# Performance work log

Hardware: AMD Instinct MI355X
Metric: run time of the kernel (lower is better)

The kernel has to match this reference:

```python
import jax, jax.numpy as jnp
import numpy as np

K = 3
STRIDE = 1
PAD = 1
DIL = 1


def _unfold(a):
    # a: (N, C, H, W) -> patches (N, C, K*K, oH, oW), matching torch.F.unfold
    # channel-major ordering (c slowest, then kernel row, then kernel col).
    N, C, H, W = a.shape
    oH = (H + 2 * PAD - DIL * (K - 1) - 1) // STRIDE + 1
    oW = (W + 2 * PAD - DIL * (K - 1) - 1) // STRIDE + 1
    ap = jnp.pad(a, ((0, 0), (0, 0), (PAD, PAD), (PAD, PAD)))
    cols = []
    for i in range(K):
        for j in range(K):
            cols.append(ap[:, :,
                           i * DIL: i * DIL + (oH - 1) * STRIDE + 1: STRIDE,
                           j * DIL: j * DIL + (oW - 1) * STRIDE + 1: STRIDE])
    return jnp.stack(cols, axis=2)  # (N, C, K*K, oH, oW)


def setup_inputs() -> dict:
    key = jax.random.key(0)
    k1, k2, k3, k4, k5 = jax.random.split(key, 5)
    N, C, O, H, W = 4, 128, 256, 128, 128
    x = jax.random.normal(k1, (N, C, H, W), dtype=jnp.float32)
    depth = jax.random.uniform(k2, (N, 1, H, W), dtype=jnp.float32)
    camera_params = jax.random.normal(k3, (N, 4), dtype=jnp.float32)
    weight = jax.random.normal(k4, (O, C, K, K), dtype=jnp.float32) * 0.05
    bias = jax.random.normal(k5, (O,), dtype=jnp.float32) * 0.05
    return {"x": x, "depth": depth, "camera_params": camera_params,
            "weight": weight, "bias": bias}


def reference(x, depth, camera_params, weight, bias):
    # camera_params is accepted but unused, mirroring the torch module.
    O, C = weight.shape[0], weight.shape[1]
    xp = _unfold(x)        # (N, C, kk, oH, oW)
    dp = _unfold(depth)    # (N, 1, kk, oH, oW)
    w = weight.reshape(O, C, K * K)
    # depth-modulated im2col GEMM: sum_{c,p} w[o,c,p] * x_patch * d_patch
    out = jnp.einsum('ocp,ncpxy->noxy', w, xp * dp)
    return out + bias[None, :, None, None]
```

## Files before the change

### kernel.cpp

```cpp
#include <hip/hip_runtime.h>
#include <stdint.h>


#define C_IN 128
#define O_OUT 256
#define HW 128
#define NB 4
#define PADW 130

#define XD_ELEMS ((size_t)NB * PADW * PADW * C_IN)
#define XD_BYTES (XD_ELEMS * 2)
#define WT_ELEMS ((size_t)O_OUT * C_IN * 9)
#define WT_BYTES (WT_ELEMS * 2)

typedef __attribute__((ext_vector_type(8))) short short8;
typedef __attribute__((ext_vector_type(4))) float f32x4;
typedef __attribute__((ext_vector_type(2))) float f32x2;
typedef __attribute__((ext_vector_type(4))) unsigned uint4v;

__device__ __forceinline__ unsigned f2bf_bits(float f) {
  unsigned u = __builtin_bit_cast(unsigned, f);
  return (u + 0x7fffu + ((u >> 16) & 1u)) >> 16;
}

__device__ __forceinline__ void async_load16(const void* g, void* l) {
  __builtin_amdgcn_global_load_lds(
      (__attribute__((address_space(1))) void*)g,
      (__attribute__((address_space(3))) void*)l, 16, 0, 0);
}

__global__ __launch_bounds__(256) void prep_all(const float* __restrict__ x,
                                                const float* __restrict__ depth,
                                                const float* __restrict__ w,
                                                short* __restrict__ xd,
                                                short* __restrict__ wt2) {
  const int R = blockIdx.x;
  const int tid = threadIdx.x;

  if (R >= NB * HW + NB) {
    int gid = (R - (NB * HW + NB)) * 4608 + tid;
#pragma unroll
    for (int i = 0; i < 18; ++i, gid += 256) {
      const int j = gid & 7;
      const int lane = (gid >> 3) & 63;
      const int T = (gid >> 9) & 7;
      const int g2 = gid >> 12;
      const int s = g2 % 36;
      const int o0 = g2 / 36;
      const int ln = lane & 15, q = lane >> 4;
      const int o = (o0 << 7) + (T << 4) + ln;
      const int cc = s / 9;
      const int tap = s % 9;
      const int c = (cc << 5) + (q << 3) + j;
      wt2[gid] = (short)f2bf_bits(w[((size_t)o * C_IN + c) * 9 + tap]);
    }
    return;
  }

  if (R >= NB * HW) {
    const int n = R - NB * HW;
    uint4v* base0 = (uint4v*)(xd + (size_t)n * PADW * PADW * C_IN);
    uint4v* base1 = (uint4v*)(xd + ((size_t)n * PADW + (PADW - 1)) * PADW * C_IN);
    const uint4v z = {0u, 0u, 0u, 0u};
    const int per_row = PADW * C_IN * 2 / 16;
    for (int i = tid; i < per_row; i += 256) {
      base0[i] = z;
      base1[i] = z;
    }
    return;
  }

  __shared__ short s[C_IN * PADW];

  const int n = R >> 7, y = R & 127;
  const int lane = tid & 63;
  const int wave = tid >> 6;

  {
    unsigned* row = (unsigned*)(xd + ((size_t)(n * PADW + y + 1) * PADW) * C_IN);
    if (tid < 64) row[tid] = 0u;
    else if (tid < 128) row[(size_t)(PADW - 1) * 64 + (tid - 64)] = 0u;
  }

  const f32x2 d2 = *(const f32x2*)(depth + ((size_t)n * HW + y) * HW + 2 * lane);
  const float* xrow = x + (((size_t)n * C_IN) * HW + y) * HW + 2 * lane;
  unsigned* s32 = (unsigned*)s;
#pragma unroll 8
  for (int ci = 0; ci < 32; ++ci) {
    const int c = ci * 4 + wave;
    const f32x2 v = *(const f32x2*)(xrow + (size_t)c * HW * HW);
    s32[c * 65 + lane] = f2bf_bits(v.x * d2.x) | (f2bf_bits(v.y * d2.y) << 16);
  }
  __syncthreads();

  const unsigned short* s16 = (const unsigned short*)s;
  unsigned* orow = (unsigned*)(xd + ((size_t)(n * PADW + y + 1) * PADW + 1) * C_IN);
#pragma unroll 8
  for (int i = 0; i < 32; ++i) {
    const int flat = tid + i * 256;
    const int px = flat >> 6, cp = flat & 63;
    const unsigned lo = s16[(2 * cp) * PADW + px];
    const unsigned hi = s16[(2 * cp + 1) * PADW + px];
    orow[flat] = lo | (hi << 16);
  }
}

__global__ __launch_bounds__(256, 2) void conv_mfma(
    const short* __restrict__ xd, const short* __restrict__ wt2,
    const float* __restrict__ bias, float* __restrict__ out) {
  __shared__ __align__(16) short xbuf[2][16640];

  const int tid = threadIdx.x;
  const int bx = blockIdx.x;
  const int n = bx >> 6;
  const int y = (bx & 63) << 1;
  const int o0b = blockIdx.y;
  const int lane = tid & 63;
  const int wave = tid >> 6;
  const int wm = wave & 1, wn = wave >> 1;
  const int ln = lane & 15, q = lane >> 4;

  const short* wbase = wt2 + (size_t)o0b * 147456 + (wm << 11) + (lane << 3);

  const short* xsrc0 = xd + (size_t)(n * PADW + y) * PADW * C_IN +
                       (tid >> 2) * C_IN + ((tid & 3) ^ ((tid >> 3) & 3)) * 8;

  f32x4 acc[4][8] = {};
  short8 areg[2][4];

  auto loadA = [&](int s, int p) {
#pragma unroll
    for (int t = 0; t < 4; ++t)
      areg[p][t] = *(const short8*)(wbase + (size_t)s * 4096 + t * 512);
  };

  {
    short* xdst = &xbuf[0][0] + tid * 8;
#pragma unroll
    for (int j = 0; j < 8; ++j)
      async_load16(xsrc0 + j * 8192, xdst + j * 2048);
    if (tid < 32) async_load16(xsrc0 + 8 * 8192, xdst + 8 * 2048);
  }
  loadA(0, 0);
  __syncthreads();

#pragma unroll
  for (int cc = 0; cc < 4; ++cc) {
#pragma unroll
    for (int tap = 0; tap < 9; ++tap) {
      const int s = cc * 9 + tap;
      if (s + 1 < 36) loadA(s + 1, (s + 1) & 1);

      if (cc + 1 < 4) {
        const short* sp = xsrc0 + ((cc + 1) << 5);
        short* xdst = &xbuf[(cc + 1) & 1][0] + tid * 8;
        if (tap < 8) async_load16(sp + tap * 8192, xdst + tap * 2048);
        if (tap == 0 && tid < 32)
          async_load16(sp + 8 * 8192, xdst + 8 * 2048);
      }

      const int ti = tap / 3, tj = tap % 3;
      const int rbase = (wn + ti) * 130 + tj;

      short8 b[8];
#pragma unroll
      for (int u = 0; u < 8; ++u) {
        const int px = rbase + (u << 4) + ln;
        const int qx = (q ^ ((px >> 1) & 3)) << 3;
        b[u] = *(const short8*)(&xbuf[cc & 1][0] + px * 32 + qx);
      }
      __builtin_amdgcn_s_setprio(1);
#pragma unroll
      for (int t = 0; t < 4; ++t)
#pragma unroll
        for (int u = 0; u < 8; ++u)
          acc[t][u] = __builtin_amdgcn_mfma_f32_16x16x32_bf16(
              areg[s & 1][t], b[u], acc[t][u], 0, 0, 0);
      __builtin_amdgcn_s_setprio(0);
    }
    if (cc + 1 < 4) __syncthreads();
  }

  const int yrow = y + wn;
#pragma unroll
  for (int t = 0; t < 4; ++t) {
    const int ob = (o0b << 7) + (wm << 6) + (t << 4) + (q << 2);
#pragma unroll
    for (int u = 0; u < 8; ++u) {
      const int xcol = (u << 4) + ln;
#pragma unroll
      for (int r = 0; r < 4; ++r) {
        const int o = ob + r;
        out[(((size_t)n * O_OUT + o) * HW + yrow) * HW + xcol] =
            acc[t][u][r] + bias[o];
      }
    }
  }
}

__global__ void conv_naive(const float* __restrict__ x,
                           const float* __restrict__ depth,
                           const float* __restrict__ w,
                           const float* __restrict__ bias,
                           float* __restrict__ out) {
  const int gid = blockIdx.x * 256 + threadIdx.x;
  if (gid >= NB * O_OUT * HW * HW) return;
  const int xc = gid & 127;
  const int y = (gid >> 7) & 127;
  const int o = (gid >> 14) & 255;
  const int n = gid >> 22;
  float s = bias[o];
  for (int c = 0; c < C_IN; ++c)
    for (int i = 0; i < 3; ++i) {
      const int yy = y + i - 1;
      if (yy < 0 || yy >= HW) continue;
      for (int j = 0; j < 3; ++j) {
        const int xx = xc + j - 1;
        if (xx < 0 || xx >= HW) continue;
        s += w[((o * C_IN + c) * 3 + i) * 3 + j] *
             x[(((size_t)n * C_IN + c) * HW + yy) * HW + xx] *
             depth[((size_t)n * HW + yy) * HW + xx];
      }
    }
  out[gid] = s;
}

extern "C" void kernel_launch(void* const* d_in, const int* in_sizes, int n_in,
                              void* d_out, int out_size, void* d_ws, size_t ws_size,
                              hipStream_t stream) {
  const float* x = (const float*)d_in[0];
  const float* depth = (const float*)d_in[1];
  const float* weight = (const float*)d_in[3];
  const float* bias = (const float*)d_in[4];
  float* out = (float*)d_out;

  const size_t need = XD_BYTES + WT_BYTES;
  if (ws_size < need) {
    conv_naive<<<(NB * O_OUT * HW * HW + 255) / 256, 256, 0, stream>>>(
        x, depth, weight, bias, out);
    return;
  }

  short* xd = (short*)d_ws;
  short* wt2 = (short*)((char*)d_ws + XD_BYTES);

  prep_all<<<NB * HW + NB + 64, 256, 0, stream>>>(x, depth, weight, xd, wt2);
  conv_mfma<<<dim3(NB * HW / 2, 2), 256, 0, stream>>>(xd, wt2, bias, out);
}
```

Measured before the change: 132.8 us.

## Split conv tile along width to halve per-block pixels and raise occupancy

Each conv block now covers 64 output columns instead of 128, giving twice as many blocks with half the LDS staging buffer and half the accumulators. Launch bounds move to 3 blocks per SM, and the staging is restructured into four padded rows plus a small tail load. The goal is more resident waves to hide latency. The cost is that each weight fragment is reused over half as many pixels, so weight traffic per output doubles.

```diff
diff --git a/kernel.cpp b/kernel.cpp
--- a/kernel.cpp
+++ b/kernel.cpp
@@ -105,15 +105,18 @@
   }
 }
 
-__global__ __launch_bounds__(256, 2) void conv_mfma(
+__global__ __launch_bounds__(256, 3) void conv_mfma(
     const short* __restrict__ xd, const short* __restrict__ wt2,
     const float* __restrict__ bias, float* __restrict__ out) {
-  __shared__ __align__(16) short xbuf[2][16640];
+  __shared__ __align__(16) short xbuf[2][8448];
 
   const int tid = threadIdx.x;
   const int bx = blockIdx.x;
-  const int n = bx >> 6;
-  const int y = (bx & 63) << 1;
+  const int n = bx >> 7;
+  const int yp = (bx >> 1) & 63;
+  const int xh = bx & 1;
+  const int y = yp << 1;
+  const int x0 = xh << 6;
   const int o0b = blockIdx.y;
   const int lane = tid & 63;
   const int wave = tid >> 6;
@@ -122,10 +125,12 @@
 
   const short* wbase = wt2 + (size_t)o0b * 147456 + (wm << 11) + (lane << 3);
 
-  const short* xsrc0 = xd + (size_t)(n * PADW + y) * PADW * C_IN +
-                       (tid >> 2) * C_IN + ((tid & 3) ^ ((tid >> 3) & 3)) * 8;
-
-  f32x4 acc[4][8] = {};
+  const short* xsrc0 = xd + ((size_t)(n * PADW + y) * PADW + x0 + (tid >> 2)) * C_IN +
+                       ((tid & 3) ^ ((tid >> 3) & 3)) * 8;
+  const short* xsrcT = xd + ((size_t)(n * PADW + y) * PADW + x0 + 64 + (tid >> 2)) * C_IN +
+                       (tid & 3) * 8;
+
+  f32x4 acc[4][4] = {};
   short8 areg[2][4];
 
   auto loadA = [&](int s, int p) {
@@ -133,13 +138,23 @@
     for (int t = 0; t < 4; ++t)
       areg[p][t] = *(const short8*)(wbase + (size_t)s * 4096 + t * 512);
   };
+  auto stageRow = [&](int cc, int b, int r) {
+    async_load16(xsrc0 + (cc << 5) + r * (PADW * C_IN),
+                 &xbuf[b][0] + tid * 8 + r * 2112);
+  };
+  auto stageTail = [&](int cc, int b) {
+    if (tid < 8) {
+#pragma unroll
+      for (int r = 0; r < 4; ++r)
+        async_load16(xsrcT + (cc << 5) + r * (PADW * C_IN),
+                     &xbuf[b][0] + r * 2112 + 2048 + tid * 8);
+    }
+  };
 
   {
-    short* xdst = &xbuf[0][0] + tid * 8;
-#pragma unroll
-    for (int j = 0; j < 8; ++j)
-      async_load16(xsrc0 + j * 8192, xdst + j * 2048);
-    if (tid < 32) async_load16(xsrc0 + 8 * 8192, xdst + 8 * 2048);
+#pragma unroll
+    for (int r = 0; r < 4; ++r) stageRow(0, 0, r);
+    stageTail(0, 0);
   }
   loadA(0, 0);
   __syncthreads();
@@ -152,28 +167,25 @@
       if (s + 1 < 36) loadA(s + 1, (s + 1) & 1);
 
       if (cc + 1 < 4) {
-        const short* sp = xsrc0 + ((cc + 1) << 5);
-        short* xdst = &xbuf[(cc + 1) & 1][0] + tid * 8;
-        if (tap < 8) async_load16(sp + tap * 8192, xdst + tap * 2048);
-        if (tap == 0 && tid < 32)
-          async_load16(sp + 8 * 8192, xdst + 8 * 2048);
+        if (tap < 4) stageRow(cc + 1, (cc + 1) & 1, tap);
+        else if (tap == 4) stageTail(cc + 1, (cc + 1) & 1);
       }
 
       const int ti = tap / 3, tj = tap % 3;
-      const int rbase = (wn + ti) * 130 + tj;
-
-      short8 b[8];
-#pragma unroll
-      for (int u = 0; u < 8; ++u) {
-        const int px = rbase + (u << 4) + ln;
-        const int qx = (q ^ ((px >> 1) & 3)) << 3;
-        b[u] = *(const short8*)(&xbuf[cc & 1][0] + px * 32 + qx);
-      }
+      const int row_s = wn + ti;
+      const int pl0 = tj + ln;
+      const int kq = (q ^ ((pl0 >> 1) & 3)) << 3;
+      const short* bb = &xbuf[cc & 1][0] + row_s * 2112 + pl0 * 32 + kq;
+
+      short8 b[4];
+#pragma unroll
+      for (int u = 0; u < 4; ++u)
+        b[u] = *(const short8*)(bb + (u << 9));
       __builtin_amdgcn_s_setprio(1);
 #pragma unroll
       for (int t = 0; t < 4; ++t)
 #pragma unroll
-        for (int u = 0; u < 8; ++u)
+        for (int u = 0; u < 4; ++u)
           acc[t][u] = __builtin_amdgcn_mfma_f32_16x16x32_bf16(
               areg[s & 1][t], b[u], acc[t][u], 0, 0, 0);
       __builtin_amdgcn_s_setprio(0);
@@ -186,8 +198,8 @@
   for (int t = 0; t < 4; ++t) {
     const int ob = (o0b << 7) + (wm << 6) + (t << 4) + (q << 2);
 #pragma unroll
-    for (int u = 0; u < 8; ++u) {
-      const int xcol = (u << 4) + ln;
+    for (int u = 0; u < 4; ++u) {
+      const int xcol = x0 + (u << 4) + ln;
 #pragma unroll
       for (int r = 0; r < 4; ++r) {
         const int o = ob + r;
@@ -245,5 +257,5 @@
   short* wt2 = (short*)((char*)d_ws + XD_BYTES);
 
   prep_all<<<NB * HW + NB + 64, 256, 0, stream>>>(x, depth, weight, xd, wt2);
-  conv_mfma<<<dim3(NB * HW / 2, 2), 256, 0, stream>>>(xd, wt2, bias, out);
-}
+  conv_mfma<<<dim3(NB * HW, 2), 256, 0, stream>>>(xd, wt2, bias, out);
+}
```

New measurement: 134.8 us. Within noise of the previous version (+1.5%).
